# Performance work log

Measured on AMD Instinct MI355X. Metric: run time of the kernel, lower is better.

Reference implementation:

```python
import jax, jax.numpy as jnp
import numpy as np

B, T, NIN = 32, 2048, 2
H, E, M = 256, 256, 64  # hidden, embed, attention model_dim
L = 256                  # max_output_len


def setup_inputs() -> dict:
    key = jax.random.key(0)
    ks = jax.random.split(key, 20)
    s = 0.05
    sl = jnp.sort(jax.random.randint(ks[1], (B,), 1, T + 1))[::-1]
    sl = sl.at[0].set(T)  # assert: seq_lens[0] == max_seq_len
    return {
        "sequence": jax.random.normal(ks[0], (B, T, NIN), dtype=jnp.float32),
        "seq_lens": sl.astype(jnp.int32),
        "max_output_len": L,
        # encoder input projection (Linear n_in->embed)
        "Wp": jax.random.normal(ks[2], (NIN, E)) * s,
        "bp": jnp.zeros((E,), jnp.float32),
        # encoder LSTM (torch gate order i,f,g,o)
        "W_ih_e": jax.random.normal(ks[3], (4 * H, E)) * s,
        "W_hh_e": jax.random.normal(ks[4], (4 * H, H)) * s,
        "b_ih_e": jnp.zeros((4 * H,), jnp.float32),
        "b_hh_e": jnp.zeros((4 * H,), jnp.float32),
        # decoder LSTMCell (input is previous hidden, size H)
        "W_ih_d": jax.random.normal(ks[5], (4 * H, H)) * s,
        "W_hh_d": jax.random.normal(ks[6], (4 * H, H)) * s,
        "b_ih_d": jnp.zeros((4 * H,), jnp.float32),
        "b_hh_d": jnp.zeros((4 * H,), jnp.float32),
        # scaled dot attention projections (d_q->model_dim, d_k->model_dim)
        "Wq": jax.random.normal(ks[7], (H, M)) * s,
        "bq": jnp.zeros((M,), jnp.float32),
        "Wk": jax.random.normal(ks[8], (H, M)) * s,
        "bk": jnp.zeros((M,), jnp.float32),
    }


def _lstm_cell(h, c, x, W_ih, W_hh, b_ih, b_hh):
    g = x @ W_ih.T + h @ W_hh.T + b_ih + b_hh  # [B,4H]
    i, f, gg, o = jnp.split(g, 4, axis=-1)
    c = jax.nn.sigmoid(f) * c + jax.nn.sigmoid(i) * jnp.tanh(gg)
    h = jax.nn.sigmoid(o) * jnp.tanh(c)
    return h, c


def reference(sequence, seq_lens, max_output_len, Wp, bp,
              W_ih_e, W_hh_e, b_ih_e, b_hh_e,
              W_ih_d, W_hh_d, b_ih_d, b_hh_d,
              Wq, bq, Wk, bk):
    b, t, _ = sequence.shape
    emb = sequence @ Wp + bp  # [B,T,E]

    # encoder LSTM over time (packed semantics recovered below)
    def estep(carry, x_t):
        h, c = carry
        h, c = _lstm_cell(h, c, x_t, W_ih_e, W_hh_e, b_ih_e, b_hh_e)
        return (h, c), (h, c)

    h0 = jnp.zeros((b, H), sequence.dtype)
    _, (hs, cs) = jax.lax.scan(estep, (h0, h0), emb.transpose(1, 0, 2))  # [T,B,H]

    valid = jnp.arange(t)[None, :] < seq_lens[:, None]  # [B,T]
    enc = hs.transpose(1, 0, 2) * valid[..., None]  # pad_packed zeros beyond seq_len
    bidx = jnp.arange(b)
    hT = hs[seq_lens - 1, bidx]  # final hidden at each seq's last valid step
    cT = cs[seq_lens - 1, bidx]

    # decoder: precompute K projection and mask bias (constant across steps)
    kproj = enc @ Wk + bk  # [B,T,M]
    bias = jnp.where(valid, 0.0, -1e9).astype(sequence.dtype)  # [B,T]
    scale = 1.0 / jnp.sqrt(jnp.asarray(M, sequence.dtype))

    def dstep(carry, _):
        h, c = carry
        h2, c2 = _lstm_cell(h, c, h, W_ih_d, W_hh_d, b_ih_d, b_hh_d)
        q = h2 @ Wq + bq  # [B,M]
        scores = jnp.einsum('bm,btm->bt', q, kproj) * scale + bias
        probs = jax.nn.softmax(scores, axis=-1)  # [B,T]
        return (h2, c2), probs

    _, ptrs = jax.lax.scan(dstep, (hT, cT), None, length=max_output_len)  # [L,B,T]
    return ptrs.transpose(1, 0, 2)  # [B,L,T]
```

## Files before the change

kernel.cpp:

```cpp
#include <hip/hip_runtime.h>
#include <stdint.h>

#define B_ 32
#define T_ 2048
#define H_ 256
#define M_ 64
#define L_ 256
#define G4_ 1024

#define NG_ 8
#define NSL_ 16
#define EPT_ 16
#define RING_ 8

__device__ __forceinline__ float sig_fast(float x){ return 1.f/(1.f+__expf(-x)); }
__device__ __forceinline__ float tanh_fast(float x){ return 2.f/(1.f+__expf(-2.f*x)) - 1.f; }
__device__ __forceinline__ float dot4(float4 a, float4 b){
  return fmaf(a.x,b.x, fmaf(a.y,b.y, fmaf(a.z,b.z, a.w*b.w)));
}

__global__ void prep_wdc(const float* __restrict__ a, const float* __restrict__ b,
                         float* __restrict__ o){
  int i = blockIdx.x*256 + threadIdx.x;
  o[i] = a[i] + b[i];
}

__global__ void prep_small(const float* __restrict__ Wp, const float* __restrict__ bp,
                           const float* __restrict__ Wihe, const float* __restrict__ bihe,
                           const float* __restrict__ bhhe, const float* __restrict__ bihd,
                           const float* __restrict__ bhhd, const float* __restrict__ Wq,
                           float* __restrict__ Wc0, float* __restrict__ Wc1,
                           float* __restrict__ bc, float* __restrict__ bdc,
                           float* __restrict__ WqT){
  int idx = blockIdx.x*256 + threadIdx.x;
  if (idx < 16384){
    int m = idx >> 8, k = idx & 255;
    WqT[m*256 + k] = Wq[k*64 + m];
  } else if (idx < 16384 + 1024){
    int j = idx - 16384;
    const float* wr = Wihe + j*256;
    float a0=0.f, a1=0.f, ab=0.f;
    for (int e=0;e<256;e++){
      float w = wr[e];
      a0 = fmaf(Wp[e],     w, a0);
      a1 = fmaf(Wp[256+e], w, a1);
      ab = fmaf(bp[e],     w, ab);
    }
    Wc0[j] = a0; Wc1[j] = a1;
    bc[j]  = ab + bihe[j] + bhhe[j];
    bdc[j] = bihd[j] + bhhd[j];
  }
}

__global__ __launch_bounds__(1024) void enc_kernel(
    const float* __restrict__ seq, const int* __restrict__ slen,
    const float* __restrict__ Whh,
    const float* __restrict__ Wc0, const float* __restrict__ Wc1,
    const float* __restrict__ bc,
    float* __restrict__ h_all, float* __restrict__ cT,
    unsigned long long* __restrict__ ring)
{
  const int tid = threadIdx.x;
  const int grp = blockIdx.x & 7, slice = blockIdx.x >> 3;
  const int rp = tid >> 4, kc = tid & 15;
  const int j = ((rp >> 4) << 8) + slice*EPT_ + (rp & 15);
  float4 w0 = *(const float4*)(Whh + (size_t)j*256 +   0 + kc*4);
  float4 w1 = *(const float4*)(Whh + (size_t)j*256 +  64 + kc*4);
  float4 w2 = *(const float4*)(Whh + (size_t)j*256 + 128 + kc*4);
  float4 w3 = *(const float4*)(Whh + (size_t)j*256 + 192 + kc*4);
  float c0 = Wc0[j], c1 = Wc1[j], cbv = bc[j];

  __shared__ float hbuf[4][256];
  __shared__ float sbuf[4][2];
  __shared__ float gbuf[4][64];

  const int ub = tid >> 4, ue = tid & 15;
  float creg = 0.f;
  int myb = 0, mylen = -1;
  if (tid < 64){ myb = grp + 8*ub; mylen = slen[myb]; }

  const int ib = tid >> 8, ik = tid & 255;
  unsigned long long* ringg = ring + (size_t)grp * (RING_*1024);

  for (int t = 0; t < T_; ++t){
    if (t == 0){
      hbuf[ib][ik] = 0.f;
    } else {
      const unsigned long long* pp = ringg + (size_t)((t-1) & (RING_-1))*1024 + tid;
      unsigned long long v;
      do { v = __hip_atomic_load(pp, __ATOMIC_RELAXED, __HIP_MEMORY_SCOPE_AGENT); }
      while ((unsigned)(v >> 32) != (unsigned)t);
      hbuf[ib][ik] = __uint_as_float((unsigned)v);
    }
    if (tid < 8) sbuf[tid>>1][tid&1] = seq[((size_t)(grp + 8*(tid>>1))*T_ + t)*2 + (tid&1)];
    __syncthreads();

#pragma unroll
    for (int i = 0; i < 4; ++i){
      float4 h0 = *(const float4*)&hbuf[i][       kc*4];
      float4 h1 = *(const float4*)&hbuf[i][ 64 + kc*4];
      float4 h2 = *(const float4*)&hbuf[i][128 + kc*4];
      float4 h3 = *(const float4*)&hbuf[i][192 + kc*4];
      float a = dot4(w0,h0) + dot4(w1,h1) + dot4(w2,h2) + dot4(w3,h3);
#pragma unroll
      for (int off = 1; off < 16; off <<= 1) a += __shfl_xor(a, off);
      if (kc == 0)
        gbuf[i][rp] = fmaf(sbuf[i][0], c0, fmaf(sbuf[i][1], c1, a + cbv));
    }
    __syncthreads();

    if (tid < 64){
      float gi = gbuf[ub][      ue];
      float gf = gbuf[ub][16 + ue];
      float gg = gbuf[ub][32 + ue];
      float go = gbuf[ub][48 + ue];
      creg = sig_fast(gf)*creg + sig_fast(gi)*tanh_fast(gg);
      float h = sig_fast(go)*tanh_fast(creg);
      unsigned long long pk = ((unsigned long long)(unsigned)(t+1) << 32)
                            | (unsigned long long)__float_as_uint(h);
      __hip_atomic_store(ringg + (size_t)(t & (RING_-1))*1024 + ub*256 + slice*EPT_ + ue,
                         pk, __ATOMIC_RELAXED, __HIP_MEMORY_SCOPE_AGENT);
      h_all[((size_t)t*B_ + myb)*H_ + slice*EPT_ + ue] = h;
      if (t == mylen - 1) cT[myb*H_ + slice*EPT_ + ue] = creg;
    }
  }
}

__global__ __launch_bounds__(1024) void dec_kernel(
    const int* __restrict__ slen,
    const float* __restrict__ Wdc, const float* __restrict__ bdc,
    const float* __restrict__ h_all, const float* __restrict__ cT,
    float* __restrict__ h2_all, unsigned long long* __restrict__ ring)
{
  const int tid = threadIdx.x;
  const int grp = blockIdx.x & 7, slice = blockIdx.x >> 3;
  const int rp = tid >> 4, kc = tid & 15;
  const int j = ((rp >> 4) << 8) + slice*EPT_ + (rp & 15);
  float4 w0 = *(const float4*)(Wdc + (size_t)j*256 +   0 + kc*4);
  float4 w1 = *(const float4*)(Wdc + (size_t)j*256 +  64 + kc*4);
  float4 w2 = *(const float4*)(Wdc + (size_t)j*256 + 128 + kc*4);
  float4 w3 = *(const float4*)(Wdc + (size_t)j*256 + 192 + kc*4);
  float cbv = bdc[j];

  __shared__ float hbuf[4][256];
  __shared__ float gbuf[4][64];

  const int ub = tid >> 4, ue = tid & 15;
  float creg = 0.f; int myb = 0;
  if (tid < 64){ myb = grp + 8*ub; creg = cT[myb*H_ + slice*EPT_ + ue]; }

  const int tb = tid >> 7, kp = tid & 127;
  const int stage_b = grp + 8*tb;
  int stage_len = 1;
  if (tid < 512) stage_len = slen[stage_b];

  const int ib = tid >> 8, ik = tid & 255;
  unsigned long long* ringg = ring + (size_t)grp * (RING_*1024);

  for (int s = 0; s < L_; ++s){
    if (s == 0){
      if (tid < 512)
        *(float2*)&hbuf[tb][kp*2] =
            *(const float2*)(h_all + ((size_t)(stage_len-1)*B_ + stage_b)*H_ + kp*2);
    } else {
      const unsigned long long* pp = ringg + (size_t)((s-1) & (RING_-1))*1024 + tid;
      unsigned long long v;
      do { v = __hip_atomic_load(pp, __ATOMIC_RELAXED, __HIP_MEMORY_SCOPE_AGENT); }
      while ((unsigned)(v >> 32) != (unsigned)s);
      hbuf[ib][ik] = __uint_as_float((unsigned)v);
    }
    __syncthreads();

#pragma unroll
    for (int i = 0; i < 4; ++i){
      float4 h0 = *(const float4*)&hbuf[i][       kc*4];
      float4 h1 = *(const float4*)&hbuf[i][ 64 + kc*4];
      float4 h2 = *(const float4*)&hbuf[i][128 + kc*4];
      float4 h3 = *(const float4*)&hbuf[i][192 + kc*4];
      float a = dot4(w0,h0) + dot4(w1,h1) + dot4(w2,h2) + dot4(w3,h3);
#pragma unroll
      for (int off = 1; off < 16; off <<= 1) a += __shfl_xor(a, off);
      if (kc == 0) gbuf[i][rp] = a + cbv;
    }
    __syncthreads();

    if (tid < 64){
      float gi = gbuf[ub][      ue];
      float gf = gbuf[ub][16 + ue];
      float gg = gbuf[ub][32 + ue];
      float go = gbuf[ub][48 + ue];
      creg = sig_fast(gf)*creg + sig_fast(gi)*tanh_fast(gg);
      float h = sig_fast(go)*tanh_fast(creg);
      unsigned long long pk = ((unsigned long long)(unsigned)(s+1) << 32)
                            | (unsigned long long)__float_as_uint(h);
      __hip_atomic_store(ringg + (size_t)(s & (RING_-1))*1024 + ub*256 + slice*EPT_ + ue,
                         pk, __ATOMIC_RELAXED, __HIP_MEMORY_SCOPE_AGENT);
      h2_all[((size_t)s*B_ + myb)*H_ + slice*EPT_ + ue] = h;
    }
  }
}

__global__ __launch_bounds__(256) void kproj_kernel(
    const float* __restrict__ h_all, const int* __restrict__ slen,
    const float* __restrict__ Wk, const float* __restrict__ bk,
    float* __restrict__ kp)
{
  __shared__ float wk[256*64];
  const int tid = threadIdx.x;
  const int b = blockIdx.x >> 4, tc = blockIdx.x & 15;
  const int t0 = tc*128;
#pragma unroll
  for (int i=0;i<16;i++){
    int idx = tid + i*256;
    *(float4*)(&wk[idx*4]) = *(const float4*)(Wk + idx*4);
  }
  __syncthreads();
  const int tp = tid>>2, mc = (tid&3)*16;
  const int ta = t0 + tp*2, tb = ta+1;
  const int len = slen[b];
  const bool va = ta < len, vb = tb < len;
  const float* ha = h_all + ((size_t)ta*B_ + b)*H_;
  const float* hb = h_all + ((size_t)tb*B_ + b)*H_;
  float4 A[4], Bv[4];
#pragma unroll
  for (int u=0;u<4;u++){ A[u].x=A[u].y=A[u].z=A[u].w=0.f; Bv[u]=A[u]; }

  for (int k4=0;k4<64;k4++){
    float xa[4], xb_[4];
    if (va){ float4 v = *(const float4*)(ha + k4*4); xa[0]=v.x; xa[1]=v.y; xa[2]=v.z; xa[3]=v.w; }
    else   { xa[0]=xa[1]=xa[2]=xa[3]=0.f; }
    if (vb){ float4 v = *(const float4*)(hb + k4*4); xb_[0]=v.x; xb_[1]=v.y; xb_[2]=v.z; xb_[3]=v.w; }
    else   { xb_[0]=xb_[1]=xb_[2]=xb_[3]=0.f; }
#pragma unroll
    for (int jj=0;jj<4;jj++){
      const float* wr = &wk[(k4*4+jj)*64 + mc];
#pragma unroll
      for (int u=0;u<4;u++){
        float4 wv = *(const float4*)(wr + u*4);
        A[u].x  = fmaf(xa[jj],wv.x,A[u].x);  A[u].y  = fmaf(xa[jj],wv.y,A[u].y);
        A[u].z  = fmaf(xa[jj],wv.z,A[u].z);  A[u].w  = fmaf(xa[jj],wv.w,A[u].w);
        Bv[u].x = fmaf(xb_[jj],wv.x,Bv[u].x); Bv[u].y = fmaf(xb_[jj],wv.y,Bv[u].y);
        Bv[u].z = fmaf(xb_[jj],wv.z,Bv[u].z); Bv[u].w = fmaf(xb_[jj],wv.w,Bv[u].w);
      }
    }
  }
#pragma unroll
  for (int u=0;u<4;u++){
    float4 bkv = *(const float4*)(bk + mc + u*4);
    float4 ra, rb;
    ra.x = va ? A[u].x+bkv.x : bkv.x;  ra.y = va ? A[u].y+bkv.y : bkv.y;
    ra.z = va ? A[u].z+bkv.z : bkv.z;  ra.w = va ? A[u].w+bkv.w : bkv.w;
    rb.x = vb ? Bv[u].x+bkv.x : bkv.x; rb.y = vb ? Bv[u].y+bkv.y : bkv.y;
    rb.z = vb ? Bv[u].z+bkv.z : bkv.z; rb.w = vb ? Bv[u].w+bkv.w : bkv.w;
    *(float4*)(kp + ((size_t)b*T_+ta)*M_ + mc + u*4) = ra;
    *(float4*)(kp + ((size_t)b*T_+tb)*M_ + mc + u*4) = rb;
  }
}

__global__ __launch_bounds__(256) void attn_kernel(
    const float* __restrict__ h2_all, const float* __restrict__ kp,
    const float* __restrict__ WqT, const float* __restrict__ bq,
    const int* __restrict__ slen, float* __restrict__ out)
{
  const int tid = threadIdx.x;
  const int b = blockIdx.x >> 5, scg = blockIdx.x & 31;
  const int s0 = scg*8;
  __shared__ float qL[8][64];
  __shared__ float red[8][4];
  const int wid = tid>>6, lane = tid&63;

  {
    const int jj = tid>>5, mh = tid&31;
    const float* hr = h2_all + ((size_t)(s0+jj)*B_ + b)*H_;
    const float* wa = WqT + (size_t)mh*256;
    const float* wb = WqT + (size_t)(mh+32)*256;
    float a0=0.f, a1=0.f;
    for (int k4=0;k4<64;k4++){
      float4 h4 = *(const float4*)(hr + k4*4);
      float4 v0 = *(const float4*)(wa + k4*4);
      float4 v1 = *(const float4*)(wb + k4*4);
      a0 += dot4(h4,v0);
      a1 += dot4(h4,v1);
    }
    qL[jj][mh]    = a0 + bq[mh];
    qL[jj][mh+32] = a1 + bq[mh+32];
  }
  __syncthreads();

  const int len = slen[b];
  float sc_[8][8];
#pragma unroll
  for (int ti=0; ti<8; ti++){
    const int t = ti*256 + tid;
    const float* kr = kp + ((size_t)b*T_ + t)*M_;
    float tmp[8];
#pragma unroll
    for (int jj=0;jj<8;jj++) tmp[jj]=0.f;
#pragma unroll
    for (int u4=0; u4<4; u4++){
      float4 k0 = *(const float4*)(kr + u4*16);
      float4 k1 = *(const float4*)(kr + u4*16 + 4);
      float4 k2 = *(const float4*)(kr + u4*16 + 8);
      float4 k3 = *(const float4*)(kr + u4*16 + 12);
#pragma unroll
      for (int jj=0;jj<8;jj++){
        const float4* q4 = (const float4*)&qL[jj][u4*16];
        tmp[jj] += dot4(k0,q4[0]) + dot4(k1,q4[1]) + dot4(k2,q4[2]) + dot4(k3,q4[3]);
      }
    }
    float bias = (t<len) ? 0.f : -1e9f;
#pragma unroll
    for (int jj=0;jj<8;jj++) sc_[ti][jj] = fmaf(tmp[jj], 0.125f, bias);
  }

  float mx[8];
#pragma unroll
  for (int jj=0;jj<8;jj++){
    float m = sc_[0][jj];
#pragma unroll
    for (int ti=1;ti<8;ti++) m = fmaxf(m, sc_[ti][jj]);
#pragma unroll
    for (int off=1; off<64; off<<=1) m = fmaxf(m, __shfl_xor(m, off));
    if (lane==0) red[jj][wid] = m;
  }
  __syncthreads();
#pragma unroll
  for (int jj=0;jj<8;jj++)
    mx[jj] = fmaxf(fmaxf(red[jj][0],red[jj][1]), fmaxf(red[jj][2],red[jj][3]));
  __syncthreads();
#pragma unroll
  for (int jj=0;jj<8;jj++){
    float s = 0.f;
#pragma unroll
    for (int ti=0;ti<8;ti++){
      float e = __expf(sc_[ti][jj] - mx[jj]);
      sc_[ti][jj] = e;
      s += e;
    }
#pragma unroll
    for (int off=1; off<64; off<<=1) s += __shfl_xor(s, off);
    if (lane==0) red[jj][wid] = s;
  }
  __syncthreads();
#pragma unroll
  for (int jj=0;jj<8;jj++){
    float r = 1.f/(red[jj][0]+red[jj][1]+red[jj][2]+red[jj][3]);
    float* o = out + ((size_t)b*L_ + s0 + jj)*T_;
#pragma unroll
    for (int ti=0;ti<8;ti++) o[ti*256 + tid] = sc_[ti][jj]*r;
  }
}

extern "C" void kernel_launch(void* const* d_in, const int* in_sizes, int n_in,
                              void* d_out, int out_size, void* d_ws, size_t ws_size,
                              hipStream_t stream) {
  (void)in_sizes; (void)n_in; (void)out_size;
  const float* seq  = (const float*)d_in[0];
  const int*   slen = (const int*)  d_in[1];
  const float* Wp   = (const float*)d_in[3];
  const float* bp   = (const float*)d_in[4];
  const float* Wihe = (const float*)d_in[5];
  const float* Whhe = (const float*)d_in[6];
  const float* bihe = (const float*)d_in[7];
  const float* bhhe = (const float*)d_in[8];
  const float* Wihd = (const float*)d_in[9];
  const float* Whhd = (const float*)d_in[10];
  const float* bihd = (const float*)d_in[11];
  const float* bhhd = (const float*)d_in[12];
  const float* Wq   = (const float*)d_in[13];
  const float* bq   = (const float*)d_in[14];
  const float* Wk   = (const float*)d_in[15];
  const float* bk   = (const float*)d_in[16];
  float* out = (float*)d_out;

  char* p = (char*)d_ws;
  auto take = [&](size_t bytes)->char* {
    char* r = p; p += (bytes + 255) & ~(size_t)255; return r;
  };
  float* h2_all = (float*)take((size_t)L_*B_*H_*4);
  float* kproj  = (float*)take((size_t)B_*T_*M_*4);
  float* cT     = (float*)take((size_t)B_*H_*4);
  float* W_dc   = (float*)take((size_t)G4_*H_*4);
  float* Wc0    = (float*)take(G4_*4);
  float* Wc1    = (float*)take(G4_*4);
  float* bc     = (float*)take(G4_*4);
  float* b_dc   = (float*)take(G4_*4);
  float* WqT    = (float*)take((size_t)M_*H_*4);
  unsigned long long* ring_e = (unsigned long long*)take((size_t)NG_*RING_*1024*8);
  unsigned long long* ring_d = (unsigned long long*)take((size_t)NG_*RING_*1024*8);

  size_t used = (size_t)(p - (char*)d_ws);
  float* h_all;
  if (ws_size >= used + (size_t)T_*B_*H_*4) {
    h_all = (float*)take((size_t)T_*B_*H_*4);
  } else {
    h_all = out;
  }

  hipMemsetAsync(ring_e, 0, (size_t)NG_*RING_*1024*8, stream);
  hipMemsetAsync(ring_d, 0, (size_t)NG_*RING_*1024*8, stream);

  prep_wdc  <<<G4_*H_/256, 256, 0, stream>>>(Wihd, Whhd, W_dc);
  prep_small<<<68, 256, 0, stream>>>(Wp, bp, Wihe, bihe, bhhe, bihd, bhhd, Wq,
                                     Wc0, Wc1, bc, b_dc, WqT);
  enc_kernel<<<NG_*NSL_, 1024, 0, stream>>>(seq, slen, Whhe, Wc0, Wc1, bc,
                                            h_all, cT, ring_e);
  kproj_kernel<<<B_*16, 256, 0, stream>>>(h_all, slen, Wk, bk, kproj);
  dec_kernel<<<NG_*NSL_, 1024, 0, stream>>>(slen, W_dc, b_dc, h_all, cT,
                                            h2_all, ring_d);
  attn_kernel<<<B_*32, 256, 0, stream>>>(h2_all, kproj, WqT, bq, slen, out);
}
```

Baseline: 6.796 ms.

## Fuse K-projection into decoder kernel to overlap it with the recurrent loop

Merges the two prep kernels into one launch, and merges the K-projection kernel into the decoder kernel as 32 extra blocks that run alongside the 128 spin-waiting decoder blocks. The aim is to hide the K-projection time behind the latency-bound decoder recurrence and to save launch overheads. The trade-off is that every decoder block now reserves 64KB of shared memory for wk, which it never uses. The decoder's spin-wait also depends on all 128 decoder blocks being co-resident, and the extra blocks may compete with them for CU resources.

```diff
diff --git a/kernel.cpp b/kernel.cpp
--- a/kernel.cpp
+++ b/kernel.cpp
@@ -12,6 +12,7 @@
 #define NSL_ 16
 #define EPT_ 16
 #define RING_ 8
+#define NDEC_ 128
 
 __device__ __forceinline__ float sig_fast(float x){ return 1.f/(1.f+__expf(-x)); }
 __device__ __forceinline__ float tanh_fast(float x){ return 2.f/(1.f+__expf(-2.f*x)) - 1.f; }
@@ -19,20 +20,22 @@
   return fmaf(a.x,b.x, fmaf(a.y,b.y, fmaf(a.z,b.z, a.w*b.w)));
 }
 
-__global__ void prep_wdc(const float* __restrict__ a, const float* __restrict__ b,
-                         float* __restrict__ o){
-  int i = blockIdx.x*256 + threadIdx.x;
-  o[i] = a[i] + b[i];
-}
-
-__global__ void prep_small(const float* __restrict__ Wp, const float* __restrict__ bp,
-                           const float* __restrict__ Wihe, const float* __restrict__ bihe,
-                           const float* __restrict__ bhhe, const float* __restrict__ bihd,
-                           const float* __restrict__ bhhd, const float* __restrict__ Wq,
-                           float* __restrict__ Wc0, float* __restrict__ Wc1,
-                           float* __restrict__ bc, float* __restrict__ bdc,
-                           float* __restrict__ WqT){
-  int idx = blockIdx.x*256 + threadIdx.x;
+__global__ void prep_all(const float* __restrict__ Wihd, const float* __restrict__ Whhd,
+                         float* __restrict__ Wdc,
+                         const float* __restrict__ Wp, const float* __restrict__ bp,
+                         const float* __restrict__ Wihe, const float* __restrict__ bihe,
+                         const float* __restrict__ bhhe, const float* __restrict__ bihd,
+                         const float* __restrict__ bhhd, const float* __restrict__ Wq,
+                         float* __restrict__ Wc0, float* __restrict__ Wc1,
+                         float* __restrict__ bc, float* __restrict__ bdc,
+                         float* __restrict__ WqT){
+  const int bid = blockIdx.x;
+  if (bid < 1024){
+    int i = bid*256 + threadIdx.x;
+    Wdc[i] = Wihd[i] + Whhd[i];
+    return;
+  }
+  int idx = (bid - 1024)*256 + threadIdx.x;
   if (idx < 16384){
     int m = idx >> 8, k = idx & 255;
     WqT[m*256 + k] = Wq[k*64 + m];
@@ -126,134 +129,137 @@
   }
 }
 
-__global__ __launch_bounds__(1024) void dec_kernel(
+__global__ __launch_bounds__(1024) void dec_kproj_kernel(
     const int* __restrict__ slen,
     const float* __restrict__ Wdc, const float* __restrict__ bdc,
     const float* __restrict__ h_all, const float* __restrict__ cT,
-    float* __restrict__ h2_all, unsigned long long* __restrict__ ring)
-{
-  const int tid = threadIdx.x;
-  const int grp = blockIdx.x & 7, slice = blockIdx.x >> 3;
-  const int rp = tid >> 4, kc = tid & 15;
-  const int j = ((rp >> 4) << 8) + slice*EPT_ + (rp & 15);
-  float4 w0 = *(const float4*)(Wdc + (size_t)j*256 +   0 + kc*4);
-  float4 w1 = *(const float4*)(Wdc + (size_t)j*256 +  64 + kc*4);
-  float4 w2 = *(const float4*)(Wdc + (size_t)j*256 + 128 + kc*4);
-  float4 w3 = *(const float4*)(Wdc + (size_t)j*256 + 192 + kc*4);
-  float cbv = bdc[j];
-
-  __shared__ float hbuf[4][256];
-  __shared__ float gbuf[4][64];
-
-  const int ub = tid >> 4, ue = tid & 15;
-  float creg = 0.f; int myb = 0;
-  if (tid < 64){ myb = grp + 8*ub; creg = cT[myb*H_ + slice*EPT_ + ue]; }
-
-  const int tb = tid >> 7, kp = tid & 127;
-  const int stage_b = grp + 8*tb;
-  int stage_len = 1;
-  if (tid < 512) stage_len = slen[stage_b];
-
-  const int ib = tid >> 8, ik = tid & 255;
-  unsigned long long* ringg = ring + (size_t)grp * (RING_*1024);
-
-  for (int s = 0; s < L_; ++s){
-    if (s == 0){
-      if (tid < 512)
-        *(float2*)&hbuf[tb][kp*2] =
-            *(const float2*)(h_all + ((size_t)(stage_len-1)*B_ + stage_b)*H_ + kp*2);
-    } else {
-      const unsigned long long* pp = ringg + (size_t)((s-1) & (RING_-1))*1024 + tid;
-      unsigned long long v;
-      do { v = __hip_atomic_load(pp, __ATOMIC_RELAXED, __HIP_MEMORY_SCOPE_AGENT); }
-      while ((unsigned)(v >> 32) != (unsigned)s);
-      hbuf[ib][ik] = __uint_as_float((unsigned)v);
-    }
-    __syncthreads();
-
-#pragma unroll
-    for (int i = 0; i < 4; ++i){
-      float4 h0 = *(const float4*)&hbuf[i][       kc*4];
-      float4 h1 = *(const float4*)&hbuf[i][ 64 + kc*4];
-      float4 h2 = *(const float4*)&hbuf[i][128 + kc*4];
-      float4 h3 = *(const float4*)&hbuf[i][192 + kc*4];
-      float a = dot4(w0,h0) + dot4(w1,h1) + dot4(w2,h2) + dot4(w3,h3);
-#pragma unroll
-      for (int off = 1; off < 16; off <<= 1) a += __shfl_xor(a, off);
-      if (kc == 0) gbuf[i][rp] = a + cbv;
-    }
-    __syncthreads();
-
-    if (tid < 64){
-      float gi = gbuf[ub][      ue];
-      float gf = gbuf[ub][16 + ue];
-      float gg = gbuf[ub][32 + ue];
-      float go = gbuf[ub][48 + ue];
-      creg = sig_fast(gf)*creg + sig_fast(gi)*tanh_fast(gg);
-      float h = sig_fast(go)*tanh_fast(creg);
-      unsigned long long pk = ((unsigned long long)(unsigned)(s+1) << 32)
-                            | (unsigned long long)__float_as_uint(h);
-      __hip_atomic_store(ringg + (size_t)(s & (RING_-1))*1024 + ub*256 + slice*EPT_ + ue,
-                         pk, __ATOMIC_RELAXED, __HIP_MEMORY_SCOPE_AGENT);
-      h2_all[((size_t)s*B_ + myb)*H_ + slice*EPT_ + ue] = h;
-    }
-  }
-}
-
-__global__ __launch_bounds__(256) void kproj_kernel(
-    const float* __restrict__ h_all, const int* __restrict__ slen,
+    float* __restrict__ h2_all, unsigned long long* __restrict__ ring,
     const float* __restrict__ Wk, const float* __restrict__ bk,
     float* __restrict__ kp)
 {
+  const int bid = blockIdx.x;
+  const int tid = threadIdx.x;
+
+  __shared__ float hbuf[4][256];
+  __shared__ float gbuf[4][64];
   __shared__ float wk[256*64];
-  const int tid = threadIdx.x;
-  const int b = blockIdx.x >> 4, tc = blockIdx.x & 15;
-  const int t0 = tc*128;
-#pragma unroll
-  for (int i=0;i<16;i++){
-    int idx = tid + i*256;
-    *(float4*)(&wk[idx*4]) = *(const float4*)(Wk + idx*4);
-  }
-  __syncthreads();
-  const int tp = tid>>2, mc = (tid&3)*16;
-  const int ta = t0 + tp*2, tb = ta+1;
-  const int len = slen[b];
-  const bool va = ta < len, vb = tb < len;
-  const float* ha = h_all + ((size_t)ta*B_ + b)*H_;
-  const float* hb = h_all + ((size_t)tb*B_ + b)*H_;
-  float4 A[4], Bv[4];
-#pragma unroll
-  for (int u=0;u<4;u++){ A[u].x=A[u].y=A[u].z=A[u].w=0.f; Bv[u]=A[u]; }
-
-  for (int k4=0;k4<64;k4++){
-    float xa[4], xb_[4];
-    if (va){ float4 v = *(const float4*)(ha + k4*4); xa[0]=v.x; xa[1]=v.y; xa[2]=v.z; xa[3]=v.w; }
-    else   { xa[0]=xa[1]=xa[2]=xa[3]=0.f; }
-    if (vb){ float4 v = *(const float4*)(hb + k4*4); xb_[0]=v.x; xb_[1]=v.y; xb_[2]=v.z; xb_[3]=v.w; }
-    else   { xb_[0]=xb_[1]=xb_[2]=xb_[3]=0.f; }
-#pragma unroll
-    for (int jj=0;jj<4;jj++){
-      const float* wr = &wk[(k4*4+jj)*64 + mc];
+
+  if (bid < NDEC_){
+    const int grp = bid & 7, slice = bid >> 3;
+    const int rp = tid >> 4, kc = tid & 15;
+    const int j = ((rp >> 4) << 8) + slice*EPT_ + (rp & 15);
+    float4 w0 = *(const float4*)(Wdc + (size_t)j*256 +   0 + kc*4);
+    float4 w1 = *(const float4*)(Wdc + (size_t)j*256 +  64 + kc*4);
+    float4 w2 = *(const float4*)(Wdc + (size_t)j*256 + 128 + kc*4);
+    float4 w3 = *(const float4*)(Wdc + (size_t)j*256 + 192 + kc*4);
+    float cbv = bdc[j];
+
+    const int ub = tid >> 4, ue = tid & 15;
+    float creg = 0.f; int myb = 0;
+    if (tid < 64){ myb = grp + 8*ub; creg = cT[myb*H_ + slice*EPT_ + ue]; }
+
+    const int tb = tid >> 7, kpp = tid & 127;
+    const int stage_b = grp + 8*tb;
+    int stage_len = 1;
+    if (tid < 512) stage_len = slen[stage_b];
+
+    const int ib = tid >> 8, ik = tid & 255;
+    unsigned long long* ringg = ring + (size_t)grp * (RING_*1024);
+
+    for (int s = 0; s < L_; ++s){
+      if (s == 0){
+        if (tid < 512)
+          *(float2*)&hbuf[tb][kpp*2] =
+              *(const float2*)(h_all + ((size_t)(stage_len-1)*B_ + stage_b)*H_ + kpp*2);
+      } else {
+        const unsigned long long* pp = ringg + (size_t)((s-1) & (RING_-1))*1024 + tid;
+        unsigned long long v;
+        do { v = __hip_atomic_load(pp, __ATOMIC_RELAXED, __HIP_MEMORY_SCOPE_AGENT); }
+        while ((unsigned)(v >> 32) != (unsigned)s);
+        hbuf[ib][ik] = __uint_as_float((unsigned)v);
+      }
+      __syncthreads();
+
+#pragma unroll
+      for (int i = 0; i < 4; ++i){
+        float4 h0 = *(const float4*)&hbuf[i][       kc*4];
+        float4 h1 = *(const float4*)&hbuf[i][ 64 + kc*4];
+        float4 h2 = *(const float4*)&hbuf[i][128 + kc*4];
+        float4 h3 = *(const float4*)&hbuf[i][192 + kc*4];
+        float a = dot4(w0,h0) + dot4(w1,h1) + dot4(w2,h2) + dot4(w3,h3);
+#pragma unroll
+        for (int off = 1; off < 16; off <<= 1) a += __shfl_xor(a, off);
+        if (kc == 0) gbuf[i][rp] = a + cbv;
+      }
+      __syncthreads();
+
+      if (tid < 64){
+        float gi = gbuf[ub][      ue];
+        float gf = gbuf[ub][16 + ue];
+        float gg = gbuf[ub][32 + ue];
+        float go = gbuf[ub][48 + ue];
+        creg = sig_fast(gf)*creg + sig_fast(gi)*tanh_fast(gg);
+        float h = sig_fast(go)*tanh_fast(creg);
+        unsigned long long pk = ((unsigned long long)(unsigned)(s+1) << 32)
+                              | (unsigned long long)__float_as_uint(h);
+        __hip_atomic_store(ringg + (size_t)(s & (RING_-1))*1024 + ub*256 + slice*EPT_ + ue,
+                           pk, __ATOMIC_RELAXED, __HIP_MEMORY_SCOPE_AGENT);
+        h2_all[((size_t)s*B_ + myb)*H_ + slice*EPT_ + ue] = h;
+      }
+    }
+  } else {
+    const int b = bid - NDEC_;
+#pragma unroll
+    for (int i=0;i<4;i++){
+      int idx = tid + i*1024;
+      *(float4*)(&wk[idx*4]) = *(const float4*)(Wk + idx*4);
+    }
+    __syncthreads();
+    const int lane = tid & 255, q = tid >> 8;
+    const int tp = lane >> 2, mc = (lane & 3)*16;
+    const int len = slen[b];
+
+    for (int it = 0; it < 4; ++it){
+      const int t0 = (it*4 + q)*128;
+      const int ta = t0 + tp*2, tb2 = ta+1;
+      const bool va = ta < len, vb = tb2 < len;
+      const float* ha = h_all + ((size_t)ta*B_ + b)*H_;
+      const float* hb = h_all + ((size_t)tb2*B_ + b)*H_;
+      float4 A[4], Bv[4];
+#pragma unroll
+      for (int u=0;u<4;u++){ A[u].x=A[u].y=A[u].z=A[u].w=0.f; Bv[u]=A[u]; }
+
+      for (int k4=0;k4<64;k4++){
+        float xa[4], xb_[4];
+        if (va){ float4 v = *(const float4*)(ha + k4*4); xa[0]=v.x; xa[1]=v.y; xa[2]=v.z; xa[3]=v.w; }
+        else   { xa[0]=xa[1]=xa[2]=xa[3]=0.f; }
+        if (vb){ float4 v = *(const float4*)(hb + k4*4); xb_[0]=v.x; xb_[1]=v.y; xb_[2]=v.z; xb_[3]=v.w; }
+        else   { xb_[0]=xb_[1]=xb_[2]=xb_[3]=0.f; }
+#pragma unroll
+        for (int jj=0;jj<4;jj++){
+          const float* wr = &wk[(k4*4+jj)*64 + mc];
+#pragma unroll
+          for (int u=0;u<4;u++){
+            float4 wv = *(const float4*)(wr + u*4);
+            A[u].x  = fmaf(xa[jj],wv.x,A[u].x);  A[u].y  = fmaf(xa[jj],wv.y,A[u].y);
+            A[u].z  = fmaf(xa[jj],wv.z,A[u].z);  A[u].w  = fmaf(xa[jj],wv.w,A[u].w);
+            Bv[u].x = fmaf(xb_[jj],wv.x,Bv[u].x); Bv[u].y = fmaf(xb_[jj],wv.y,Bv[u].y);
+            Bv[u].z = fmaf(xb_[jj],wv.z,Bv[u].z); Bv[u].w = fmaf(xb_[jj],wv.w,Bv[u].w);
+          }
+        }
+      }
 #pragma unroll
       for (int u=0;u<4;u++){
-        float4 wv = *(const float4*)(wr + u*4);
-        A[u].x  = fmaf(xa[jj],wv.x,A[u].x);  A[u].y  = fmaf(xa[jj],wv.y,A[u].y);
-        A[u].z  = fmaf(xa[jj],wv.z,A[u].z);  A[u].w  = fmaf(xa[jj],wv.w,A[u].w);
-        Bv[u].x = fmaf(xb_[jj],wv.x,Bv[u].x); Bv[u].y = fmaf(xb_[jj],wv.y,Bv[u].y);
-        Bv[u].z = fmaf(xb_[jj],wv.z,Bv[u].z); Bv[u].w = fmaf(xb_[jj],wv.w,Bv[u].w);
-      }
-    }
-  }
-#pragma unroll
-  for (int u=0;u<4;u++){
-    float4 bkv = *(const float4*)(bk + mc + u*4);
-    float4 ra, rb;
-    ra.x = va ? A[u].x+bkv.x : bkv.x;  ra.y = va ? A[u].y+bkv.y : bkv.y;
-    ra.z = va ? A[u].z+bkv.z : bkv.z;  ra.w = va ? A[u].w+bkv.w : bkv.w;
-    rb.x = vb ? Bv[u].x+bkv.x : bkv.x; rb.y = vb ? Bv[u].y+bkv.y : bkv.y;
-    rb.z = vb ? Bv[u].z+bkv.z : bkv.z; rb.w = vb ? Bv[u].w+bkv.w : bkv.w;
-    *(float4*)(kp + ((size_t)b*T_+ta)*M_ + mc + u*4) = ra;
-    *(float4*)(kp + ((size_t)b*T_+tb)*M_ + mc + u*4) = rb;
+        float4 bkv = *(const float4*)(bk + mc + u*4);
+        float4 ra, rb;
+        ra.x = va ? A[u].x+bkv.x : bkv.x;  ra.y = va ? A[u].y+bkv.y : bkv.y;
+        ra.z = va ? A[u].z+bkv.z : bkv.z;  ra.w = va ? A[u].w+bkv.w : bkv.w;
+        rb.x = vb ? Bv[u].x+bkv.x : bkv.x; rb.y = vb ? Bv[u].y+bkv.y : bkv.y;
+        rb.z = vb ? Bv[u].z+bkv.z : bkv.z; rb.w = vb ? Bv[u].w+bkv.w : bkv.w;
+        *(float4*)(kp + ((size_t)b*T_+ta)*M_ + mc + u*4) = ra;
+        *(float4*)(kp + ((size_t)b*T_+tb2)*M_ + mc + u*4) = rb;
+      }
+    }
   }
 }
 
@@ -400,13 +406,12 @@
   hipMemsetAsync(ring_e, 0, (size_t)NG_*RING_*1024*8, stream);
   hipMemsetAsync(ring_d, 0, (size_t)NG_*RING_*1024*8, stream);
 
-  prep_wdc  <<<G4_*H_/256, 256, 0, stream>>>(Wihd, Whhd, W_dc);
-  prep_small<<<68, 256, 0, stream>>>(Wp, bp, Wihe, bihe, bhhe, bihd, bhhd, Wq,
-                                     Wc0, Wc1, bc, b_dc, WqT);
+  prep_all<<<1024 + 68, 256, 0, stream>>>(Wihd, Whhd, W_dc,
+                                          Wp, bp, Wihe, bihe, bhhe, bihd, bhhd, Wq,
+                                          Wc0, Wc1, bc, b_dc, WqT);
   enc_kernel<<<NG_*NSL_, 1024, 0, stream>>>(seq, slen, Whhe, Wc0, Wc1, bc,
                                             h_all, cT, ring_e);
-  kproj_kernel<<<B_*16, 256, 0, stream>>>(h_all, slen, Wk, bk, kproj);
-  dec_kernel<<<NG_*NSL_, 1024, 0, stream>>>(slen, W_dc, b_dc, h_all, cT,
-                                            h2_all, ring_d);
+  dec_kproj_kernel<<<NDEC_ + B_, 1024, 0, stream>>>(slen, W_dc, b_dc, h_all, cT,
+                                                    h2_all, ring_d, Wk, bk, kproj);
   attn_kernel<<<B_*32, 256, 0, stream>>>(h2_all, kproj, WqT, bq, slen, out);
 }
```

New measurement: 6.752 ms. No clear change (-0.6%).
